# Kernel tuning notes

Hardware: AMD Instinct MI355X
Metric: run time of the kernel (lower is better)

Reference implementation:

```python
import jax, jax.numpy as jnp
import numpy as np

N_QUBITS = 4
DIM = 2 ** N_QUBITS  # 16-dim statevector
KERNEL = 3
STRIDE = 1
PADDING = 1


def _rot_mats(w):
    # PennyLane Rot(phi, theta, omega) = RZ(omega) RY(theta) RZ(phi)
    phi, theta, omega = w[:, 0], w[:, 1], w[:, 2]
    c = jnp.cos(theta / 2)
    s = jnp.sin(theta / 2)
    em = jnp.exp(-0.5j * (phi + omega))
    ep = jnp.exp(0.5j * (phi + omega))
    ed = jnp.exp(0.5j * (phi - omega))
    edm = jnp.exp(-0.5j * (phi - omega))
    row0 = jnp.stack([em * c, -ed * s], axis=-1)
    row1 = jnp.stack([edm * s, ep * c], axis=-1)
    return jnp.stack([row0, row1], axis=-2)  # [n_qubits, 2, 2]


def _apply_1q(state, U, wire):
    # state: [M] + [2]*n, wire axis is 1+wire (wire 0 is most significant)
    s = jnp.moveaxis(state, 1 + wire, -1)
    s = jnp.einsum('...b,ab->...a', s, U)
    return jnp.moveaxis(s, -1, 1 + wire)


def _apply_cnot(state, c, t):
    s = jnp.moveaxis(state, (1 + c, 1 + t), (-2, -1))
    shp = s.shape
    s = s.reshape(shp[:-2] + (4,))[..., jnp.array([0, 1, 3, 2])].reshape(shp)
    return jnp.moveaxis(s, (-2, -1), (1 + c, 1 + t))


def _forward(x, W_pre, b_pre, W_post, b_post, q_weights):
    B, C, L = x.shape
    xp = jnp.pad(x, ((0, 0), (0, 0), (PADDING, PADDING)))
    L_out = (L + 2 * PADDING - KERNEL) // STRIDE + 1
    starts = jnp.arange(L_out) * STRIDE
    # windows: [B, C, L_out, K] -> flatten channel-major like torch reshape
    win = xp[:, :, starts[:, None] + jnp.arange(KERNEL)[None, :]]
    win = win.transpose(0, 2, 1, 3).reshape(B, L_out, C * KERNEL)
    pre = win @ W_pre.T + b_pre  # [B, L_out, n_qubits]
    # AmplitudeEmbedding: pad to 2**n and normalize
    v = jnp.pad(pre, ((0, 0), (0, 0), (0, DIM - N_QUBITS)))
    v = v / jnp.linalg.norm(v, axis=-1, keepdims=True)
    state = v.reshape(B * L_out, *([2] * N_QUBITS)).astype(jnp.complex64)
    U = _rot_mats(q_weights)
    for i in range(N_QUBITS):
        state = _apply_1q(state, U[i], i)
    for i in range(N_QUBITS - 1):
        state = _apply_cnot(state, i, i + 1)
    flat = state.reshape(B * L_out, DIM)
    probs = jnp.real(flat) ** 2 + jnp.imag(flat) ** 2
    # PauliZ expectation per wire: sign of bit i (wire 0 = MSB)
    bits = (jnp.arange(DIM)[None, :] >> (N_QUBITS - 1 - jnp.arange(N_QUBITS)[:, None])) & 1
    z = (1 - 2 * bits).astype(probs.dtype)  # [n_qubits, DIM]
    expz = (probs @ z.T).reshape(B, L_out, N_QUBITS)
    out = expz @ W_post.T + b_post  # [B, L_out, out_channels]
    return out.transpose(0, 2, 1)


def setup_inputs() -> dict:
    key = jax.random.key(0)
    ks = jax.random.split(key, 6)
    B, C, L = 32, 80, 3000
    OUT = 512
    return {
        'x': jax.random.normal(ks[0], (B, C, L), dtype=jnp.float32),
        'W_pre': jax.random.normal(ks[1], (N_QUBITS, C * KERNEL), dtype=jnp.float32) * 0.06,
        'b_pre': jax.random.normal(ks[2], (N_QUBITS,), dtype=jnp.float32) * 0.06,
        'W_post': jax.random.normal(ks[3], (OUT, N_QUBITS), dtype=jnp.float32) * 0.4,
        'b_post': jax.random.normal(ks[4], (OUT,), dtype=jnp.float32) * 0.4,
        'q_weights': jax.random.normal(ks[5], (N_QUBITS, 3), dtype=jnp.float32),
    }


def reference(x, W_pre, b_pre, W_post, b_post, q_weights):
    return _forward(x, W_pre, b_pre, W_post, b_post, q_weights)
```

## Files before the change

kernel.cpp:

```cpp
#include <hip/hip_runtime.h>
#include <math.h>

#define C_IN 80
#define L_IN 3000
#define OUT_C 512
#define NT 768
#define NW 12
#define TL 192
#define CPT 20

typedef float floatx4 __attribute__((ext_vector_type(4)));

struct c2f { float x, y; };

__device__ __forceinline__ c2f cmul(c2f a, c2f b) {
    return { a.x*b.x - a.y*b.y, a.x*b.y + a.y*b.x };
}
__device__ __forceinline__ c2f csel(c2f a, c2f b, int bit) {
    c2f r; r.x = bit ? b.x : a.x; r.y = bit ? b.y : a.y; return r;
}
__device__ __forceinline__ float quadform(const float4* __restrict__ A, float4 p) {
    float4 r0 = A[0], r1 = A[1], r2 = A[2], r3 = A[3];
    return p.x*(r0.x*p.x + r0.y*p.y + r0.z*p.z + r0.w*p.w)
         + p.y*(r1.x*p.x + r1.y*p.y + r1.z*p.z + r1.w*p.w)
         + p.z*(r2.x*p.x + r2.y*p.y + r2.z*p.z + r2.w*p.w)
         + p.w*(r3.x*p.x + r3.y*p.y + r3.z*p.z + r3.w*p.w);
}

__global__ __launch_bounds__(NT) void qconv_kernel(
    const float* __restrict__ x,
    const float* __restrict__ W_pre,
    const float* __restrict__ b_pre,
    const float* __restrict__ W_post,
    const float* __restrict__ b_post,
    const float* __restrict__ qw,
    float* __restrict__ out)
{
    __shared__ float4 s_wpre[C_IN*3];
    __shared__ float4 s_post[OUT_C];
    __shared__ float  s_bpost[OUT_C];
    __shared__ float4 s_A[16];
    __shared__ float4 s_part[3][TL];
    __shared__ float4 s_e[TL];

    const int t    = threadIdx.x;
    const int w    = t >> 6;
    const int lane = t & 63;
    const int b    = blockIdx.y;
    const int l0   = blockIdx.x * TL;

    for (int i = t; i < C_IN*3; i += NT) {
        s_wpre[i] = make_float4(W_pre[0*C_IN*3 + i], W_pre[1*C_IN*3 + i],
                                W_pre[2*C_IN*3 + i], W_pre[3*C_IN*3 + i]);
    }
    if (t < OUT_C) {
        s_post[t]  = *reinterpret_cast<const float4*>(&W_post[t*4]);
        s_bpost[t] = b_post[t];
    }
    __syncthreads();

    if (t < 64) {
        c2f U[4][2][2];
        #pragma unroll
        for (int i = 0; i < 4; ++i) {
            float phi = qw[i*3+0], theta = qw[i*3+1], omega = qw[i*3+2];
            float sh, ch;  sincosf(0.5f*theta, &sh, &ch);
            float s1, c1;  sincosf(0.5f*(phi+omega), &s1, &c1);
            float s2, cv;  sincosf(0.5f*(phi-omega), &s2, &cv);
            U[i][0][0] = {  c1*ch, -s1*ch };
            U[i][0][1] = { -cv*sh, -s2*sh };
            U[i][1][0] = {  cv*sh, -s2*sh };
            U[i][1][1] = {  c1*ch,  s1*ch };
        }
        const int q  = t >> 4;
        const int j  = (t >> 2) & 3;
        const int jp = t & 3;
        const int j2  = (j  >> 1) & 1, j3  = j  & 1;
        const int jp2 = (jp >> 1) & 1, jp3 = jp & 1;
        float s = 0.f;
        #pragma unroll
        for (int k = 0; k < 16; ++k) {
            int m = k ^ ((k >> 1) & 1);
            m ^= ((m >> 2) & 1) << 1;
            m ^= ((m >> 3) & 1) << 2;
            const int m0 = (m >> 3) & 1, m1 = (m >> 2) & 1;
            const int m2 = (m >> 1) & 1, m3 = m & 1;
            c2f w01 = cmul(U[0][m0][0], U[1][m1][0]);
            c2f av = cmul(w01, cmul(csel(U[2][m2][0], U[2][m2][1], j2),
                                    csel(U[3][m3][0], U[3][m3][1], j3)));
            c2f bv = cmul(w01, cmul(csel(U[2][m2][0], U[2][m2][1], jp2),
                                    csel(U[3][m3][0], U[3][m3][1], jp3)));
            float z = 1.f - 2.f * ((k >> (3 - q)) & 1);
            s += z * (av.x*bv.x + av.y*bv.y);
        }
        ((float*)s_A)[t] = s;
    }

    const int h = w / 3;
    const int i = (w % 3) * 64 + lane;
    const int l = l0 + i;
    const bool lv = (l < L_IN);

    float4 acc = (h == 0) ? make_float4(b_pre[0], b_pre[1], b_pre[2], b_pre[3])
                          : make_float4(0.f, 0.f, 0.f, 0.f);
    if (lv) {
        const float* __restrict__ xr = x + (size_t)b * C_IN * L_IN + (size_t)(h*CPT) * L_IN + l;
        const bool hm = (l >= 1), hp = (l + 1 < L_IN);
        #pragma unroll 2
        for (int c = 0; c < CPT; ++c) {
            const float* r = xr + c * L_IN;
            float xa = hm ? r[-1] : 0.f;
            float xb = r[0];
            float xc = hp ? r[1] : 0.f;
            const int ck = (h*CPT + c) * 3;
            float4 w0 = s_wpre[ck], w1 = s_wpre[ck+1], w2 = s_wpre[ck+2];
            acc.x += w0.x*xa + w1.x*xb + w2.x*xc;
            acc.y += w0.y*xa + w1.y*xb + w2.y*xc;
            acc.z += w0.z*xa + w1.z*xb + w2.z*xc;
            acc.w += w0.w*xa + w1.w*xb + w2.w*xc;
        }
    }
    if (h > 0) s_part[h-1][i] = acc;
    __syncthreads();

    if (t < TL) {
        float4 p = acc;
        float4 p1 = s_part[0][t], p2 = s_part[1][t], p3 = s_part[2][t];
        p.x += p1.x + p2.x + p3.x;
        p.y += p1.y + p2.y + p3.y;
        p.z += p1.z + p2.z + p3.z;
        p.w += p1.w + p2.w + p3.w;
        const float inv = 1.f / (p.x*p.x + p.y*p.y + p.z*p.z + p.w*p.w);
        float4 e;
        e.x = quadform(&s_A[0],  p) * inv;
        e.y = quadform(&s_A[4],  p) * inv;
        e.z = quadform(&s_A[8],  p) * inv;
        e.w = quadform(&s_A[12], p) * inv;
        s_e[t] = e;
    }
    __syncthreads();

    if (lane < 48) {
        const int lq  = l0 + 4*lane;
        const bool sv = (lq < L_IN);
        if (sv) {
            const float4 e0 = s_e[4*lane+0];
            const float4 e1 = s_e[4*lane+1];
            const float4 e2 = s_e[4*lane+2];
            const float4 e3 = s_e[4*lane+3];
            float* op = out + ((size_t)b * OUT_C + w) * L_IN + lq;
            #pragma unroll 4
            for (int o = w; o < OUT_C; o += NW) {
                const float4 wv = s_post[o];
                const float  bb = s_bpost[o];
                floatx4 st;
                st.x = wv.x*e0.x + wv.y*e0.y + wv.z*e0.z + wv.w*e0.w + bb;
                st.y = wv.x*e1.x + wv.y*e1.y + wv.z*e1.z + wv.w*e1.w + bb;
                st.z = wv.x*e2.x + wv.y*e2.y + wv.z*e2.z + wv.w*e2.w + bb;
                st.w = wv.x*e3.x + wv.y*e3.y + wv.z*e3.z + wv.w*e3.w + bb;
                *reinterpret_cast<floatx4*>(op) = st;
                op += (size_t)NW * L_IN;
            }
        }
    }
}

extern "C" void kernel_launch(void* const* d_in, const int* in_sizes, int n_in,
                              void* d_out, int out_size, void* d_ws, size_t ws_size,
                              hipStream_t stream) {
    const float* x      = (const float*)d_in[0];
    const float* W_pre  = (const float*)d_in[1];
    const float* b_pre  = (const float*)d_in[2];
    const float* W_post = (const float*)d_in[3];
    const float* b_post = (const float*)d_in[4];
    const float* qw     = (const float*)d_in[5];
    float* out = (float*)d_out;

    const int B = in_sizes[0] / (C_IN * L_IN);
    dim3 grid((L_IN + TL - 1) / TL, B);
    qconv_kernel<<<grid, NT, 0, stream>>>(x, W_pre, b_pre, W_post, b_post, qw, out);
}
```

Before: 44.09 us.

## Process two L tiles per block, overlap conv with stores, shuffle-reduce channels

Each block now handles two 192-position tiles. The conv for the second tile is interleaved with the output stores of the first, so input loads overlap with the heavy write traffic. The channel-split reduction moves from shared memory plus a barrier to 4-lane shuffles, where each quad of lanes shares one position. Weight loading overlaps with the quantum matrix setup by giving it to the non-first waves. The trade-offs are half as many blocks (8x32 = 256, roughly one per CU) and a lower per-quad coalescing width for x loads (16 positions per wave per channel).

```diff
diff --git a/kernel.cpp b/kernel.cpp
--- a/kernel.cpp
+++ b/kernel.cpp
@@ -7,7 +7,7 @@
 #define NT 768
 #define NW 12
 #define TL 192
-#define CPT 20
+#define NTILE 2
 
 typedef float floatx4 __attribute__((ext_vector_type(4)));
 
@@ -40,24 +40,15 @@
     __shared__ float4 s_post[OUT_C];
     __shared__ float  s_bpost[OUT_C];
     __shared__ float4 s_A[16];
-    __shared__ float4 s_part[3][TL];
-    __shared__ float4 s_e[TL];
+    __shared__ float4 s_e[NTILE][TL];
 
     const int t    = threadIdx.x;
     const int w    = t >> 6;
     const int lane = t & 63;
+    const int part = lane & 3;
+    const int li   = lane >> 2;
     const int b    = blockIdx.y;
-    const int l0   = blockIdx.x * TL;
-
-    for (int i = t; i < C_IN*3; i += NT) {
-        s_wpre[i] = make_float4(W_pre[0*C_IN*3 + i], W_pre[1*C_IN*3 + i],
-                                W_pre[2*C_IN*3 + i], W_pre[3*C_IN*3 + i]);
-    }
-    if (t < OUT_C) {
-        s_post[t]  = *reinterpret_cast<const float4*>(&W_post[t*4]);
-        s_bpost[t] = b_post[t];
-    }
-    __syncthreads();
+    const int bl0  = blockIdx.x * (TL * NTILE);
 
     if (t < 64) {
         c2f U[4][2][2];
@@ -94,75 +85,86 @@
             s += z * (av.x*bv.x + av.y*bv.y);
         }
         ((float*)s_A)[t] = s;
-    }
-
-    const int h = w / 3;
-    const int i = (w % 3) * 64 + lane;
-    const int l = l0 + i;
-    const bool lv = (l < L_IN);
-
-    float4 acc = (h == 0) ? make_float4(b_pre[0], b_pre[1], b_pre[2], b_pre[3])
-                          : make_float4(0.f, 0.f, 0.f, 0.f);
-    if (lv) {
-        const float* __restrict__ xr = x + (size_t)b * C_IN * L_IN + (size_t)(h*CPT) * L_IN + l;
-        const bool hm = (l >= 1), hp = (l + 1 < L_IN);
-        #pragma unroll 2
-        for (int c = 0; c < CPT; ++c) {
-            const float* r = xr + c * L_IN;
-            float xa = hm ? r[-1] : 0.f;
-            float xb = r[0];
-            float xc = hp ? r[1] : 0.f;
-            const int ck = (h*CPT + c) * 3;
-            float4 w0 = s_wpre[ck], w1 = s_wpre[ck+1], w2 = s_wpre[ck+2];
-            acc.x += w0.x*xa + w1.x*xb + w2.x*xc;
-            acc.y += w0.y*xa + w1.y*xb + w2.y*xc;
-            acc.z += w0.z*xa + w1.z*xb + w2.z*xc;
-            acc.w += w0.w*xa + w1.w*xb + w2.w*xc;
+    } else {
+        for (int i = t - 64; i < C_IN*3; i += NT - 64) {
+            s_wpre[i] = make_float4(W_pre[0*C_IN*3 + i], W_pre[1*C_IN*3 + i],
+                                    W_pre[2*C_IN*3 + i], W_pre[3*C_IN*3 + i]);
         }
-    }
-    if (h > 0) s_part[h-1][i] = acc;
-    __syncthreads();
-
-    if (t < TL) {
-        float4 p = acc;
-        float4 p1 = s_part[0][t], p2 = s_part[1][t], p3 = s_part[2][t];
-        p.x += p1.x + p2.x + p3.x;
-        p.y += p1.y + p2.y + p3.y;
-        p.z += p1.z + p2.z + p3.z;
-        p.w += p1.w + p2.w + p3.w;
-        const float inv = 1.f / (p.x*p.x + p.y*p.y + p.z*p.z + p.w*p.w);
-        float4 e;
-        e.x = quadform(&s_A[0],  p) * inv;
-        e.y = quadform(&s_A[4],  p) * inv;
-        e.z = quadform(&s_A[8],  p) * inv;
-        e.w = quadform(&s_A[12], p) * inv;
-        s_e[t] = e;
+        for (int i = t - 64; i < OUT_C; i += NT - 64) {
+            s_post[i]  = *reinterpret_cast<const float4*>(&W_post[i*4]);
+            s_bpost[i] = b_post[i];
+        }
     }
     __syncthreads();
 
-    if (lane < 48) {
-        const int lq  = l0 + 4*lane;
-        const bool sv = (lq < L_IN);
-        if (sv) {
-            const float4 e0 = s_e[4*lane+0];
-            const float4 e1 = s_e[4*lane+1];
-            const float4 e2 = s_e[4*lane+2];
-            const float4 e3 = s_e[4*lane+3];
-            float* op = out + ((size_t)b * OUT_C + w) * L_IN + lq;
+    auto conv_q = [&](int tile) {
+        const int l = bl0 + tile*TL + w*16 + li;
+        const bool lv = (l < L_IN);
+        float4 acc = (part == 0) ? make_float4(b_pre[0], b_pre[1], b_pre[2], b_pre[3])
+                                 : make_float4(0.f, 0.f, 0.f, 0.f);
+        if (lv) {
+            const float* __restrict__ xr = x + (size_t)b * C_IN * L_IN + (size_t)(part*20) * L_IN + l;
+            const bool hm = (l >= 1), hp = (l + 1 < L_IN);
             #pragma unroll 4
-            for (int o = w; o < OUT_C; o += NW) {
-                const float4 wv = s_post[o];
-                const float  bb = s_bpost[o];
-                floatx4 st;
-                st.x = wv.x*e0.x + wv.y*e0.y + wv.z*e0.z + wv.w*e0.w + bb;
-                st.y = wv.x*e1.x + wv.y*e1.y + wv.z*e1.z + wv.w*e1.w + bb;
-                st.z = wv.x*e2.x + wv.y*e2.y + wv.z*e2.z + wv.w*e2.w + bb;
-                st.w = wv.x*e3.x + wv.y*e3.y + wv.z*e3.z + wv.w*e3.w + bb;
-                *reinterpret_cast<floatx4*>(op) = st;
-                op += (size_t)NW * L_IN;
+            for (int c = 0; c < 20; ++c) {
+                const float* r = xr + c * L_IN;
+                float xa = hm ? r[-1] : 0.f;
+                float xb = r[0];
+                float xc = hp ? r[1] : 0.f;
+                const int ck = (part*20 + c) * 3;
+                float4 w0 = s_wpre[ck], w1 = s_wpre[ck+1], w2 = s_wpre[ck+2];
+                acc.x += w0.x*xa + w1.x*xb + w2.x*xc;
+                acc.y += w0.y*xa + w1.y*xb + w2.y*xc;
+                acc.z += w0.z*xa + w1.z*xb + w2.z*xc;
+                acc.w += w0.w*xa + w1.w*xb + w2.w*xc;
             }
         }
-    }
+        acc.x += __shfl_xor(acc.x, 1); acc.x += __shfl_xor(acc.x, 2);
+        acc.y += __shfl_xor(acc.y, 1); acc.y += __shfl_xor(acc.y, 2);
+        acc.z += __shfl_xor(acc.z, 1); acc.z += __shfl_xor(acc.z, 2);
+        acc.w += __shfl_xor(acc.w, 1); acc.w += __shfl_xor(acc.w, 2);
+        const float inv = 1.f / (acc.x*acc.x + acc.y*acc.y + acc.z*acc.z + acc.w*acc.w);
+        float4 e;
+        e.x = quadform(&s_A[0],  acc) * inv;
+        e.y = quadform(&s_A[4],  acc) * inv;
+        e.z = quadform(&s_A[8],  acc) * inv;
+        e.w = quadform(&s_A[12], acc) * inv;
+        if (part == 0) s_e[tile][w*16 + li] = e;
+    };
+
+    auto store_tile = [&](int tile) {
+        if (lane < 48) {
+            const int lq = bl0 + tile*TL + 4*lane;
+            if (lq < L_IN) {
+                const float4 e0 = s_e[tile][4*lane+0];
+                const float4 e1 = s_e[tile][4*lane+1];
+                const float4 e2 = s_e[tile][4*lane+2];
+                const float4 e3 = s_e[tile][4*lane+3];
+                float* op = out + ((size_t)b * OUT_C + w) * L_IN + lq;
+                #pragma unroll 4
+                for (int o = w; o < OUT_C; o += NW) {
+                    const float4 wv = s_post[o];
+                    const float  bb = s_bpost[o];
+                    floatx4 st;
+                    st.x = wv.x*e0.x + wv.y*e0.y + wv.z*e0.z + wv.w*e0.w + bb;
+                    st.y = wv.x*e1.x + wv.y*e1.y + wv.z*e1.z + wv.w*e1.w + bb;
+                    st.z = wv.x*e2.x + wv.y*e2.y + wv.z*e2.z + wv.w*e2.w + bb;
+                    st.w = wv.x*e3.x + wv.y*e3.y + wv.z*e3.z + wv.w*e3.w + bb;
+                    *reinterpret_cast<floatx4*>(op) = st;
+                    op += (size_t)NW * L_IN;
+                }
+            }
+        }
+    };
+
+    conv_q(0);
+    __syncthreads();
+
+    store_tile(0);
+    conv_q(1);
+    __syncthreads();
+
+    store_tile(1);
 }
 
 extern "C" void kernel_launch(void* const* d_in, const int* in_sizes, int n_in,
@@ -177,6 +179,6 @@
     float* out = (float*)d_out;
 
     const int B = in_sizes[0] / (C_IN * L_IN);
-    dim3 grid((L_IN + TL - 1) / TL, B);
+    dim3 grid((L_IN + TL*NTILE - 1) / (TL*NTILE), B);
     qconv_kernel<<<grid, NT, 0, stream>>>(x, W_pre, b_pre, W_post, b_post, qw, out);
 }
```

After: 50.14 us. +13.7%, slower.

## Process two L-tiles per block and prefetch next tile's input during stores

Applied to the files above, without the earlier changes.

Each block now handles two consecutive 192-wide tiles. The second tile's input window is loaded into registers before the first tile's output stores are issued, with scheduling barriers to keep them in that order, so input reads overlap the output-store phase. It also spreads the per-block setup (weight staging and the quadratic-form matrix) over twice the work. The cost is half as many blocks, more register pressure from 60 prefetched floats per thread, and lower occupancy, in a kernel whose run time is likely dominated by output-store bandwidth.

```diff
diff --git a/kernel.cpp b/kernel.cpp
--- a/kernel.cpp
+++ b/kernel.cpp
@@ -7,6 +7,7 @@
 #define NT 768
 #define NW 12
 #define TL 192
+#define NTILE 2
 #define CPT 20
 
 typedef float floatx4 __attribute__((ext_vector_type(4)));
@@ -41,13 +42,13 @@
     __shared__ float  s_bpost[OUT_C];
     __shared__ float4 s_A[16];
     __shared__ float4 s_part[3][TL];
-    __shared__ float4 s_e[TL];
+    __shared__ float4 s_e[NTILE][TL];
 
     const int t    = threadIdx.x;
     const int w    = t >> 6;
     const int lane = t & 63;
     const int b    = blockIdx.y;
-    const int l0   = blockIdx.x * TL;
+    const int bl0  = blockIdx.x * (TL * NTILE);
 
     for (int i = t; i < C_IN*3; i += NT) {
         s_wpre[i] = make_float4(W_pre[0*C_IN*3 + i], W_pre[1*C_IN*3 + i],
@@ -98,71 +99,117 @@
 
     const int h = w / 3;
     const int i = (w % 3) * 64 + lane;
-    const int l = l0 + i;
-    const bool lv = (l < L_IN);
-
-    float4 acc = (h == 0) ? make_float4(b_pre[0], b_pre[1], b_pre[2], b_pre[3])
-                          : make_float4(0.f, 0.f, 0.f, 0.f);
-    if (lv) {
-        const float* __restrict__ xr = x + (size_t)b * C_IN * L_IN + (size_t)(h*CPT) * L_IN + l;
-        const bool hm = (l >= 1), hp = (l + 1 < L_IN);
-        #pragma unroll 2
+    const float4 bias0 = make_float4(b_pre[0], b_pre[1], b_pre[2], b_pre[3]);
+
+    auto reduce_e = [&](int tile, float4 acc) {
+        if (t < TL) {
+            float4 p = acc;
+            float4 p1 = s_part[0][t], p2 = s_part[1][t], p3 = s_part[2][t];
+            p.x += p1.x + p2.x + p3.x;
+            p.y += p1.y + p2.y + p3.y;
+            p.z += p1.z + p2.z + p3.z;
+            p.w += p1.w + p2.w + p3.w;
+            const float inv = 1.f / (p.x*p.x + p.y*p.y + p.z*p.z + p.w*p.w);
+            float4 e;
+            e.x = quadform(&s_A[0],  p) * inv;
+            e.y = quadform(&s_A[4],  p) * inv;
+            e.z = quadform(&s_A[8],  p) * inv;
+            e.w = quadform(&s_A[12], p) * inv;
+            s_e[tile][t] = e;
+        }
+    };
+
+    auto store_tile = [&](int tile) {
+        if (lane < 48) {
+            const int lq = bl0 + tile*TL + 4*lane;
+            if (lq < L_IN) {
+                const float4 e0 = s_e[tile][4*lane+0];
+                const float4 e1 = s_e[tile][4*lane+1];
+                const float4 e2 = s_e[tile][4*lane+2];
+                const float4 e3 = s_e[tile][4*lane+3];
+                float* op = out + ((size_t)b * OUT_C + w) * L_IN + lq;
+                #pragma unroll 4
+                for (int o = w; o < OUT_C; o += NW) {
+                    const float4 wv = s_post[o];
+                    const float  bb = s_bpost[o];
+                    floatx4 st;
+                    st.x = wv.x*e0.x + wv.y*e0.y + wv.z*e0.z + wv.w*e0.w + bb;
+                    st.y = wv.x*e1.x + wv.y*e1.y + wv.z*e1.z + wv.w*e1.w + bb;
+                    st.z = wv.x*e2.x + wv.y*e2.y + wv.z*e2.z + wv.w*e2.w + bb;
+                    st.w = wv.x*e3.x + wv.y*e3.y + wv.z*e3.z + wv.w*e3.w + bb;
+                    *reinterpret_cast<floatx4*>(op) = st;
+                    op += (size_t)NW * L_IN;
+                }
+            }
+        }
+    };
+
+    float4 acc0 = (h == 0) ? bias0 : make_float4(0.f, 0.f, 0.f, 0.f);
+    {
+        const int l = bl0 + i;
+        const bool lv = (l < L_IN);
+        if (lv) {
+            const float* __restrict__ xr = x + (size_t)b * C_IN * L_IN + (size_t)(h*CPT) * L_IN + l;
+            const bool hm = (l >= 1), hp = (l + 1 < L_IN);
+            #pragma unroll 2
+            for (int c = 0; c < CPT; ++c) {
+                const float* r = xr + c * L_IN;
+                float xa = hm ? r[-1] : 0.f;
+                float xb = r[0];
+                float xc = hp ? r[1] : 0.f;
+                const int ck = (h*CPT + c) * 3;
+                float4 w0 = s_wpre[ck], w1 = s_wpre[ck+1], w2 = s_wpre[ck+2];
+                acc0.x += w0.x*xa + w1.x*xb + w2.x*xc;
+                acc0.y += w0.y*xa + w1.y*xb + w2.y*xc;
+                acc0.z += w0.z*xa + w1.z*xb + w2.z*xc;
+                acc0.w += w0.w*xa + w1.w*xb + w2.w*xc;
+            }
+        }
+        if (h > 0) s_part[h-1][i] = acc0;
+    }
+    __syncthreads();
+
+    reduce_e(0, acc0);
+    __syncthreads();
+
+    float pa[CPT], pb[CPT], pc[CPT];
+    {
+        const int l1 = bl0 + TL + i;
+        const int lc = (l1 < L_IN) ? l1 : (L_IN - 2);
+        const bool hp = (l1 + 1 < L_IN);
+        const int cp = hp ? 1 : 0;
+        const float* __restrict__ xr = x + (size_t)b * C_IN * L_IN + (size_t)(h*CPT) * L_IN + lc;
+        #pragma unroll
         for (int c = 0; c < CPT; ++c) {
             const float* r = xr + c * L_IN;
-            float xa = hm ? r[-1] : 0.f;
-            float xb = r[0];
-            float xc = hp ? r[1] : 0.f;
-            const int ck = (h*CPT + c) * 3;
-            float4 w0 = s_wpre[ck], w1 = s_wpre[ck+1], w2 = s_wpre[ck+2];
-            acc.x += w0.x*xa + w1.x*xb + w2.x*xc;
-            acc.y += w0.y*xa + w1.y*xb + w2.y*xc;
-            acc.z += w0.z*xa + w1.z*xb + w2.z*xc;
-            acc.w += w0.w*xa + w1.w*xb + w2.w*xc;
-        }
-    }
-    if (h > 0) s_part[h-1][i] = acc;
-    __syncthreads();
-
-    if (t < TL) {
-        float4 p = acc;
-        float4 p1 = s_part[0][t], p2 = s_part[1][t], p3 = s_part[2][t];
-        p.x += p1.x + p2.x + p3.x;
-        p.y += p1.y + p2.y + p3.y;
-        p.z += p1.z + p2.z + p3.z;
-        p.w += p1.w + p2.w + p3.w;
-        const float inv = 1.f / (p.x*p.x + p.y*p.y + p.z*p.z + p.w*p.w);
-        float4 e;
-        e.x = quadform(&s_A[0],  p) * inv;
-        e.y = quadform(&s_A[4],  p) * inv;
-        e.z = quadform(&s_A[8],  p) * inv;
-        e.w = quadform(&s_A[12], p) * inv;
-        s_e[t] = e;
-    }
-    __syncthreads();
-
-    if (lane < 48) {
-        const int lq  = l0 + 4*lane;
-        const bool sv = (lq < L_IN);
-        if (sv) {
-            const float4 e0 = s_e[4*lane+0];
-            const float4 e1 = s_e[4*lane+1];
-            const float4 e2 = s_e[4*lane+2];
-            const float4 e3 = s_e[4*lane+3];
-            float* op = out + ((size_t)b * OUT_C + w) * L_IN + lq;
-            #pragma unroll 4
-            for (int o = w; o < OUT_C; o += NW) {
-                const float4 wv = s_post[o];
-                const float  bb = s_bpost[o];
-                floatx4 st;
-                st.x = wv.x*e0.x + wv.y*e0.y + wv.z*e0.z + wv.w*e0.w + bb;
-                st.y = wv.x*e1.x + wv.y*e1.y + wv.z*e1.z + wv.w*e1.w + bb;
-                st.z = wv.x*e2.x + wv.y*e2.y + wv.z*e2.z + wv.w*e2.w + bb;
-                st.w = wv.x*e3.x + wv.y*e3.y + wv.z*e3.z + wv.w*e3.w + bb;
-                *reinterpret_cast<floatx4*>(op) = st;
-                op += (size_t)NW * L_IN;
-            }
-        }
-    }
+            pa[c] = r[-1];
+            pb[c] = r[0];
+            float vc = r[cp];
+            pc[c] = hp ? vc : 0.f;
+        }
+    }
+    __builtin_amdgcn_sched_barrier(0);
+
+    store_tile(0);
+    __builtin_amdgcn_sched_barrier(0);
+
+    float4 acc1 = (h == 0) ? bias0 : make_float4(0.f, 0.f, 0.f, 0.f);
+    #pragma unroll
+    for (int c = 0; c < CPT; ++c) {
+        const int ck = (h*CPT + c) * 3;
+        float4 w0 = s_wpre[ck], w1 = s_wpre[ck+1], w2 = s_wpre[ck+2];
+        acc1.x += w0.x*pa[c] + w1.x*pb[c] + w2.x*pc[c];
+        acc1.y += w0.y*pa[c] + w1.y*pb[c] + w2.y*pc[c];
+        acc1.z += w0.z*pa[c] + w1.z*pb[c] + w2.z*pc[c];
+        acc1.w += w0.w*pa[c] + w1.w*pb[c] + w2.w*pc[c];
+    }
+    if (h > 0) s_part[h-1][i] = acc1;
+    __syncthreads();
+
+    reduce_e(1, acc1);
+    __syncthreads();
+
+    store_tile(1);
 }
 
 extern "C" void kernel_launch(void* const* d_in, const int* in_sizes, int n_in,
@@ -177,6 +224,6 @@
     float* out = (float*)d_out;
 
     const int B = in_sizes[0] / (C_IN * L_IN);
-    dim3 grid((L_IN + TL - 1) / TL, B);
+    dim3 grid((L_IN + TL*NTILE - 1) / (TL*NTILE), B);
     qconv_kernel<<<grid, NT, 0, stream>>>(x, W_pre, b_pre, W_post, b_post, qw, out);
 }
```

Measured after the change: 45.45 us. +3.1%, slower.
